# Kernel optimization log

Measured on AMD Instinct MI355X. Metric: run time of the kernel, lower is better.

## Reference

```python
import jax, jax.numpy as jnp
import numpy as np


def setup_inputs() -> dict:
    key = jax.random.key(0)
    ks = jax.random.split(key, 6)
    B, Tq, Tk = 4, 512, 512
    Q, K, C = 1024, 1024, 256
    query = jax.random.normal(ks[0], (B, Tq, Q), dtype=jnp.float32)
    kmat = jax.random.normal(ks[1], (B, Tk, K), dtype=jnp.float32)
    # Linear weights (torch nn.Linear stores [out, in]; we keep [in, out] for einsum)
    Wq = jax.random.normal(ks[2], (Q, C), dtype=jnp.float32) / np.sqrt(Q)
    Wk = jax.random.normal(ks[3], (K, C), dtype=jnp.float32) / np.sqrt(K)
    w_attn = jax.random.normal(ks[4], (C,), dtype=jnp.float32) / np.sqrt(C)
    b_attn = jax.random.normal(ks[5], (), dtype=jnp.float32) * 0.01
    return {"query": query, "key": kmat, "Wq": Wq, "Wk": Wk,
            "w_attn": w_attn, "b_attn": b_attn}


def reference(query, key, Wq, Wk, w_attn, b_attn):
    # Additive (Bahdanau) attention scores.
    # q2ctx: (B, Tq, C); k2ctx: (B, Tk, C)
    q2ctx = jnp.einsum('bqi,ic->bqc', query, Wq)
    k2ctx = jnp.einsum('bki,ic->bkc', key, Wk)
    # broadcast add -> (B, Tq, Tk, C), tanh, project to scalar and squeeze
    ctx = jnp.tanh(q2ctx[:, :, None, :] + k2ctx[:, None, :, :])
    scores = jnp.einsum('bqkc,c->bqk', ctx, w_attn) + b_attn
    return scores  # (B, Tq, Tk)
```

## Files before the change

kernel.cpp:

```cpp
#include <hip/hip_runtime.h>
#include <hip/hip_bf16.h>

#define M_ROWS 2048
#define KDIM   1024
#define CDIM   256
#define TQ     512
#define TK     512

#define GBM 64
#define GBN 32
#define GBK 32

#define QT 64
#define KT 32

#define SCALE2LOG2E 2.8853900817779268f

typedef __attribute__((ext_vector_type(8))) short short8;
typedef __attribute__((ext_vector_type(4))) float floatx4;
typedef __attribute__((ext_vector_type(2))) float f32x2;

__device__ __forceinline__ short2 cvt2(float x, float y) {
    __hip_bfloat162 h = __float22bfloat162_rn(make_float2(x, y));
    short2 r;
    __builtin_memcpy(&r, &h, sizeof(r));
    return r;
}

__global__ __launch_bounds__(256) void gemm_mfma_kernel(
    const float* __restrict__ Aq, const float* __restrict__ Ak,
    const float* __restrict__ Wq, const float* __restrict__ Wk,
    const float* __restrict__ w_attn,
    float* __restrict__ Eq, float* __restrict__ Ek)
{
    __shared__ short As[GBM][GBK + 8];
    __shared__ short Ws[GBN][GBK + 8];

    const int z = blockIdx.z;
    const float* A = z ? Ak : Aq;
    const float* W = z ? Wk : Wq;
    float*       E = z ? Ek : Eq;

    const int t    = threadIdx.x;
    const int lane = t & 63;
    const int wave = t >> 6;
    const int m0   = blockIdx.x * GBM;
    const int n0   = blockIdx.y * GBN;

    const int ar = t >> 2;
    const int ac = (t & 3) * 8;
    const int wr = t >> 3;
    const int wc = (t & 7) * 4;

    const int iw = wave & 1;
    const int jw = wave >> 1;
    const int li = lane & 15;
    const int qd = lane >> 4;

    floatx4 acc0 = {0.f, 0.f, 0.f, 0.f};
    floatx4 acc1 = {0.f, 0.f, 0.f, 0.f};

    float4 a0 = *(const float4*)&A[(size_t)(m0 + ar) * KDIM + ac];
    float4 a1 = *(const float4*)&A[(size_t)(m0 + ar) * KDIM + ac + 4];
    float4 w0 = *(const float4*)&W[(size_t)wr * CDIM + n0 + wc];

    for (int k0 = 0; k0 < KDIM; k0 += GBK) {
        __syncthreads();
        short2 p0 = cvt2(a0.x, a0.y), p1 = cvt2(a0.z, a0.w);
        short2 p2 = cvt2(a1.x, a1.y), p3 = cvt2(a1.z, a1.w);
        short8 av = { p0.x, p0.y, p1.x, p1.y, p2.x, p2.y, p3.x, p3.y };
        *(short8*)&As[ar][ac] = av;
        short2 u0 = cvt2(w0.x, w0.y), u1 = cvt2(w0.z, w0.w);
        Ws[wc + 0][wr] = u0.x;
        Ws[wc + 1][wr] = u0.y;
        Ws[wc + 2][wr] = u1.x;
        Ws[wc + 3][wr] = u1.y;
        __syncthreads();
        if (k0 + GBK < KDIM) {
            a0 = *(const float4*)&A[(size_t)(m0 + ar) * KDIM + k0 + GBK + ac];
            a1 = *(const float4*)&A[(size_t)(m0 + ar) * KDIM + k0 + GBK + ac + 4];
            w0 = *(const float4*)&W[(size_t)(k0 + GBK + wr) * CDIM + n0 + wc];
        }
        short8 af  = *(const short8*)&Ws[iw * 16 + li][qd * 8];
        short8 bf0 = *(const short8*)&As[jw * 32 + li][qd * 8];
        short8 bf1 = *(const short8*)&As[jw * 32 + 16 + li][qd * 8];
        acc0 = __builtin_amdgcn_mfma_f32_16x16x32_bf16(af, bf0, acc0, 0, 0, 0);
        acc1 = __builtin_amdgcn_mfma_f32_16x16x32_bf16(af, bf1, acc1, 0, 0, 0);
    }

    #pragma unroll
    for (int r = 0; r < 4; ++r) {
        const int c = n0 + iw * 16 + qd * 4 + r;
        float scale = z ? 1.0f : (-0.5f / w_attn[c]);
        float v0 = __builtin_amdgcn_exp2f(acc0[r] * SCALE2LOG2E) * scale;
        float v1 = __builtin_amdgcn_exp2f(acc1[r] * SCALE2LOG2E) * scale;
        E[(size_t)c * M_ROWS + m0 + jw * 32 + li]      = v0;
        E[(size_t)c * M_ROWS + m0 + jw * 32 + 16 + li] = v1;
    }
}

__global__ __launch_bounds__(256) void bahdanau_kernel(
    const float* __restrict__ Eqs, const float* __restrict__ Ek,
    const float* __restrict__ w_attn, const float* __restrict__ b_attn,
    float* __restrict__ out)
{
    __shared__ float qs[64][QT + 4];
    __shared__ float ks[64][KT + 4];
    __shared__ float sl[CDIM];
    __shared__ float partial[4];

    const int t  = threadIdx.x;
    const int b  = blockIdx.z;
    const int q0 = blockIdx.x * QT;
    const int k0 = blockIdx.y * KT;
    const int gq = b * TQ + q0;
    const int gk = b * TK + k0;
    const int tq = (t >> 4) * 4;
    const int tk = (t & 15) * 2;

    const int qlr = t >> 4;
    const int qlc = (t & 15) * 4;
    const int klr = t >> 3;
    const int klc = (t & 7) * 4;

    {
        float wv = w_attn[t];
        sl[t] = -0.5f / wv;
        float sum = wv;
        #pragma unroll
        for (int o = 32; o >= 1; o >>= 1) sum += __shfl_down(sum, o);
        if ((t & 63) == 0) partial[t >> 6] = sum;
    }

    float4 qv[4], kv[2];
    #pragma unroll
    for (int j = 0; j < 4; ++j)
        qv[j] = *(const float4*)&Eqs[(size_t)(qlr + 16 * j) * M_ROWS + gq + qlc];
    #pragma unroll
    for (int j = 0; j < 2; ++j)
        kv[j] = *(const float4*)&Ek[(size_t)(klr + 32 * j) * M_ROWS + gk + klc];

    f32x2 acc[4] = {{0.f, 0.f}, {0.f, 0.f}, {0.f, 0.f}, {0.f, 0.f}};

    for (int ch = 0; ch < 4; ++ch) {
        __syncthreads();
        #pragma unroll
        for (int j = 0; j < 4; ++j) *(float4*)&qs[qlr + 16 * j][qlc] = qv[j];
        #pragma unroll
        for (int j = 0; j < 2; ++j) *(float4*)&ks[klr + 32 * j][klc] = kv[j];
        __syncthreads();
        if (ch < 3) {
            const int c1 = (ch + 1) * 64;
            #pragma unroll
            for (int j = 0; j < 4; ++j)
                qv[j] = *(const float4*)&Eqs[(size_t)(c1 + qlr + 16 * j) * M_ROWS + gq + qlc];
            #pragma unroll
            for (int j = 0; j < 2; ++j)
                kv[j] = *(const float4*)&Ek[(size_t)(c1 + klr + 32 * j) * M_ROWS + gk + klc];
        }
        const int cb = ch * 64;
        #pragma unroll 4
        for (int c = 0; c < 64; c += 2) {
            float s1v = sl[cb + c], s2v = sl[cb + c + 1];
            f32x2 s1 = {s1v, s1v}, s2 = {s2v, s2v};
            float4 q1 = *(const float4*)&qs[c][tq];
            float4 q2 = *(const float4*)&qs[c + 1][tq];
            f32x2 k1 = *(const f32x2*)&ks[c][tk];
            f32x2 k2 = *(const f32x2*)&ks[c + 1][tk];
            {
                f32x2 f1 = __builtin_elementwise_fma((f32x2){q1.x, q1.x}, k1, s1);
                f32x2 f2 = __builtin_elementwise_fma((f32x2){q2.x, q2.x}, k2, s2);
                f32x2 g = f1 * f2, h = f1 + f2;
                f32x2 r = {__builtin_amdgcn_rcpf(g.x), __builtin_amdgcn_rcpf(g.y)};
                acc[0] = __builtin_elementwise_fma(h, r, acc[0]);
            }
            {
                f32x2 f1 = __builtin_elementwise_fma((f32x2){q1.y, q1.y}, k1, s1);
                f32x2 f2 = __builtin_elementwise_fma((f32x2){q2.y, q2.y}, k2, s2);
                f32x2 g = f1 * f2, h = f1 + f2;
                f32x2 r = {__builtin_amdgcn_rcpf(g.x), __builtin_amdgcn_rcpf(g.y)};
                acc[1] = __builtin_elementwise_fma(h, r, acc[1]);
            }
            {
                f32x2 f1 = __builtin_elementwise_fma((f32x2){q1.z, q1.z}, k1, s1);
                f32x2 f2 = __builtin_elementwise_fma((f32x2){q2.z, q2.z}, k2, s2);
                f32x2 g = f1 * f2, h = f1 + f2;
                f32x2 r = {__builtin_amdgcn_rcpf(g.x), __builtin_amdgcn_rcpf(g.y)};
                acc[2] = __builtin_elementwise_fma(h, r, acc[2]);
            }
            {
                f32x2 f1 = __builtin_elementwise_fma((f32x2){q1.w, q1.w}, k1, s1);
                f32x2 f2 = __builtin_elementwise_fma((f32x2){q2.w, q2.w}, k2, s2);
                f32x2 g = f1 * f2, h = f1 + f2;
                f32x2 r = {__builtin_amdgcn_rcpf(g.x), __builtin_amdgcn_rcpf(g.y)};
                acc[3] = __builtin_elementwise_fma(h, r, acc[3]);
            }
        }
    }

    const float bias2 = *b_attn + partial[0] + partial[1] + partial[2] + partial[3];
    float* o = out + ((size_t)b * TQ + q0 + tq) * TK + k0 + tk;
    #pragma unroll
    for (int i = 0; i < 4; ++i)
        *(float2*)&o[i * TK] = make_float2(acc[i].x + bias2, acc[i].y + bias2);
}

extern "C" void kernel_launch(void* const* d_in, const int* in_sizes, int n_in,
                              void* d_out, int out_size, void* d_ws, size_t ws_size,
                              hipStream_t stream) {
    const float* query  = (const float*)d_in[0];
    const float* key    = (const float*)d_in[1];
    const float* Wq     = (const float*)d_in[2];
    const float* Wk     = (const float*)d_in[3];
    const float* w_attn = (const float*)d_in[4];
    const float* b_attn = (const float*)d_in[5];
    float* out = (float*)d_out;

    float* Eqs = (float*)d_ws;
    float* Ek  = Eqs + (size_t)CDIM * M_ROWS;

    dim3 gemm_grid(M_ROWS / GBM, CDIM / GBN, 2);
    gemm_mfma_kernel<<<gemm_grid, 256, 0, stream>>>(query, key, Wq, Wk, w_attn, Eqs, Ek);

    dim3 main_grid(TQ / QT, TK / KT, 4);
    bahdanau_kernel<<<main_grid, 256, 0, stream>>>(Eqs, Ek, w_attn, b_attn, out);
}
```

Measured before the change: 124.5 us.

## Combine four reciprocal terms per rcp and shrink attention tile to 32x32

The inner loop now merges four tanh-like fractions (f1..f4) into one numerator and denominator, so it needs one reciprocal per four channels instead of one per two. The main kernel tile drops from 64x32 to 32x32 with two outputs per thread, and the grid grows to match. This targets the transcendental-unit cost of v_rcp, which dominates the pairwise loop. In exchange it adds extra multiplies, raises the risk of overflow or precision loss in a product of four terms, and loads more from LDS per output because the tile is smaller.

Measured after the change: 122.7 us. No clear change (-1.5%).

```diff
diff --git a/kernel.cpp b/kernel.cpp
--- a/kernel.cpp
+++ b/kernel.cpp
@@ -11,9 +11,6 @@
 #define GBN 32
 #define GBK 32
 
-#define QT 64
-#define KT 32
-
 #define SCALE2LOG2E 2.8853900817779268f
 
 typedef __attribute__((ext_vector_type(8))) short short8;
@@ -26,6 +23,8 @@
     __builtin_memcpy(&r, &h, sizeof(r));
     return r;
 }
+
+__device__ __forceinline__ f32x2 splat2(float x) { return (f32x2){x, x}; }
 
 __global__ __launch_bounds__(256) void gemm_mfma_kernel(
     const float* __restrict__ Aq, const float* __restrict__ Ak,
@@ -104,24 +103,22 @@
     const float* __restrict__ w_attn, const float* __restrict__ b_attn,
     float* __restrict__ out)
 {
-    __shared__ float qs[64][QT + 4];
-    __shared__ float ks[64][KT + 4];
-    __shared__ float sl[CDIM];
+    __shared__ float qs[64][36];
+    __shared__ float ks[64][36];
+    __shared__ __align__(16) float sl[CDIM];
     __shared__ float partial[4];
 
     const int t  = threadIdx.x;
     const int b  = blockIdx.z;
-    const int q0 = blockIdx.x * QT;
-    const int k0 = blockIdx.y * KT;
+    const int q0 = blockIdx.x * 32;
+    const int k0 = blockIdx.y * 32;
     const int gq = b * TQ + q0;
     const int gk = b * TK + k0;
-    const int tq = (t >> 4) * 4;
+    const int tq = (t >> 4) * 2;
     const int tk = (t & 15) * 2;
 
-    const int qlr = t >> 4;
-    const int qlc = (t & 15) * 4;
-    const int klr = t >> 3;
-    const int klc = (t & 7) * 4;
+    const int lr = t >> 3;
+    const int lc = (t & 7) * 4;
 
     {
         float wv = w_attn[t];
@@ -132,77 +129,75 @@
         if ((t & 63) == 0) partial[t >> 6] = sum;
     }
 
-    float4 qv[4], kv[2];
+    float4 qv[2], kv[2];
     #pragma unroll
-    for (int j = 0; j < 4; ++j)
-        qv[j] = *(const float4*)&Eqs[(size_t)(qlr + 16 * j) * M_ROWS + gq + qlc];
-    #pragma unroll
-    for (int j = 0; j < 2; ++j)
-        kv[j] = *(const float4*)&Ek[(size_t)(klr + 32 * j) * M_ROWS + gk + klc];
-
-    f32x2 acc[4] = {{0.f, 0.f}, {0.f, 0.f}, {0.f, 0.f}, {0.f, 0.f}};
+    for (int j = 0; j < 2; ++j) {
+        qv[j] = *(const float4*)&Eqs[(size_t)(lr + 32 * j) * M_ROWS + gq + lc];
+        kv[j] = *(const float4*)&Ek [(size_t)(lr + 32 * j) * M_ROWS + gk + lc];
+    }
+
+    f32x2 accA = {0.f, 0.f};
+    f32x2 accB = {0.f, 0.f};
 
     for (int ch = 0; ch < 4; ++ch) {
         __syncthreads();
         #pragma unroll
-        for (int j = 0; j < 4; ++j) *(float4*)&qs[qlr + 16 * j][qlc] = qv[j];
-        #pragma unroll
-        for (int j = 0; j < 2; ++j) *(float4*)&ks[klr + 32 * j][klc] = kv[j];
+        for (int j = 0; j < 2; ++j) {
+            *(float4*)&qs[lr + 32 * j][lc] = qv[j];
+            *(float4*)&ks[lr + 32 * j][lc] = kv[j];
+        }
         __syncthreads();
         if (ch < 3) {
             const int c1 = (ch + 1) * 64;
             #pragma unroll
-            for (int j = 0; j < 4; ++j)
-                qv[j] = *(const float4*)&Eqs[(size_t)(c1 + qlr + 16 * j) * M_ROWS + gq + qlc];
-            #pragma unroll
-            for (int j = 0; j < 2; ++j)
-                kv[j] = *(const float4*)&Ek[(size_t)(c1 + klr + 32 * j) * M_ROWS + gk + klc];
+            for (int j = 0; j < 2; ++j) {
+                qv[j] = *(const float4*)&Eqs[(size_t)(c1 + lr + 32 * j) * M_ROWS + gq + lc];
+                kv[j] = *(const float4*)&Ek [(size_t)(c1 + lr + 32 * j) * M_ROWS + gk + lc];
+            }
         }
         const int cb = ch * 64;
-        #pragma unroll 4
-        for (int c = 0; c < 64; c += 2) {
-            float s1v = sl[cb + c], s2v = sl[cb + c + 1];
-            f32x2 s1 = {s1v, s1v}, s2 = {s2v, s2v};
-            float4 q1 = *(const float4*)&qs[c][tq];
-            float4 q2 = *(const float4*)&qs[c + 1][tq];
-            f32x2 k1 = *(const f32x2*)&ks[c][tk];
-            f32x2 k2 = *(const f32x2*)&ks[c + 1][tk];
+        #pragma unroll
+        for (int cc = 0; cc < 64; cc += 4) {
+            float4 s4 = *(const float4*)&sl[cb + cc];
+            f32x2 q1 = *(const f32x2*)&qs[cc + 0][tq];
+            f32x2 q2 = *(const f32x2*)&qs[cc + 1][tq];
+            f32x2 q3 = *(const f32x2*)&qs[cc + 2][tq];
+            f32x2 q4 = *(const f32x2*)&qs[cc + 3][tq];
+            f32x2 k1 = *(const f32x2*)&ks[cc + 0][tk];
+            f32x2 k2 = *(const f32x2*)&ks[cc + 1][tk];
+            f32x2 k3 = *(const f32x2*)&ks[cc + 2][tk];
+            f32x2 k4 = *(const f32x2*)&ks[cc + 3][tk];
             {
-                f32x2 f1 = __builtin_elementwise_fma((f32x2){q1.x, q1.x}, k1, s1);
-                f32x2 f2 = __builtin_elementwise_fma((f32x2){q2.x, q2.x}, k2, s2);
-                f32x2 g = f1 * f2, h = f1 + f2;
-                f32x2 r = {__builtin_amdgcn_rcpf(g.x), __builtin_amdgcn_rcpf(g.y)};
-                acc[0] = __builtin_elementwise_fma(h, r, acc[0]);
+                f32x2 f1 = __builtin_elementwise_fma(splat2(q1.x), k1, splat2(s4.x));
+                f32x2 f2 = __builtin_elementwise_fma(splat2(q2.x), k2, splat2(s4.y));
+                f32x2 f3 = __builtin_elementwise_fma(splat2(q3.x), k3, splat2(s4.z));
+                f32x2 f4 = __builtin_elementwise_fma(splat2(q4.x), k4, splat2(s4.w));
+                f32x2 p12 = f1 * f2, p34 = f3 * f4;
+                f32x2 s12 = f1 + f2, s34 = f3 + f4;
+                f32x2 num = __builtin_elementwise_fma(s12, p34, s34 * p12);
+                f32x2 den = p12 * p34;
+                f32x2 r = {__builtin_amdgcn_rcpf(den.x), __builtin_amdgcn_rcpf(den.y)};
+                accA = __builtin_elementwise_fma(num, r, accA);
             }
             {
-                f32x2 f1 = __builtin_elementwise_fma((f32x2){q1.y, q1.y}, k1, s1);
-                f32x2 f2 = __builtin_elementwise_fma((f32x2){q2.y, q2.y}, k2, s2);
-                f32x2 g = f1 * f2, h = f1 + f2;
-                f32x2 r = {__builtin_amdgcn_rcpf(g.x), __builtin_amdgcn_rcpf(g.y)};
-                acc[1] = __builtin_elementwise_fma(h, r, acc[1]);
-            }
-            {
-                f32x2 f1 = __builtin_elementwise_fma((f32x2){q1.z, q1.z}, k1, s1);
-                f32x2 f2 = __builtin_elementwise_fma((f32x2){q2.z, q2.z}, k2, s2);
-                f32x2 g = f1 * f2, h = f1 + f2;
-                f32x2 r = {__builtin_amdgcn_rcpf(g.x), __builtin_amdgcn_rcpf(g.y)};
-                acc[2] = __builtin_elementwise_fma(h, r, acc[2]);
-            }
-            {
-                f32x2 f1 = __builtin_elementwise_fma((f32x2){q1.w, q1.w}, k1, s1);
-                f32x2 f2 = __builtin_elementwise_fma((f32x2){q2.w, q2.w}, k2, s2);
-                f32x2 g = f1 * f2, h = f1 + f2;
-                f32x2 r = {__builtin_amdgcn_rcpf(g.x), __builtin_amdgcn_rcpf(g.y)};
-                acc[3] = __builtin_elementwise_fma(h, r, acc[3]);
+                f32x2 f1 = __builtin_elementwise_fma(splat2(q1.y), k1, splat2(s4.x));
+                f32x2 f2 = __builtin_elementwise_fma(splat2(q2.y), k2, splat2(s4.y));
+                f32x2 f3 = __builtin_elementwise_fma(splat2(q3.y), k3, splat2(s4.z));
+                f32x2 f4 = __builtin_elementwise_fma(splat2(q4.y), k4, splat2(s4.w));
+                f32x2 p12 = f1 * f2, p34 = f3 * f4;
+                f32x2 s12 = f1 + f2, s34 = f3 + f4;
+                f32x2 num = __builtin_elementwise_fma(s12, p34, s34 * p12);
+                f32x2 den = p12 * p34;
+                f32x2 r = {__builtin_amdgcn_rcpf(den.x), __builtin_amdgcn_rcpf(den.y)};
+                accB = __builtin_elementwise_fma(num, r, accB);
             }
         }
     }
 
     const float bias2 = *b_attn + partial[0] + partial[1] + partial[2] + partial[3];
     float* o = out + ((size_t)b * TQ + q0 + tq) * TK + k0 + tk;
-    #pragma unroll
-    for (int i = 0; i < 4; ++i)
-        *(float2*)&o[i * TK] = make_float2(acc[i].x + bias2, acc[i].y + bias2);
+    *(float2*)&o[0]  = make_float2(accA.x + bias2, accA.y + bias2);
+    *(float2*)&o[TK] = make_float2(accB.x + bias2, accB.y + bias2);
 }
 
 extern "C" void kernel_launch(void* const* d_in, const int* in_sizes, int n_in,
@@ -222,6 +217,6 @@
     dim3 gemm_grid(M_ROWS / GBM, CDIM / GBN, 2);
     gemm_mfma_kernel<<<gemm_grid, 256, 0, stream>>>(query, key, Wq, Wk, w_attn, Eqs, Ek);
 
-    dim3 main_grid(TQ / QT, TK / KT, 4);
+    dim3 main_grid(TQ / 32, TK / 32, 4);
     bahdanau_kernel<<<main_grid, 256, 0, stream>>>(Eqs, Ek, w_attn, b_attn, out);
 }
```
